# Kernel optimization log

Hardware: AMD Instinct MI355X
Metric: run time of the kernel (lower is better)

Reference implementation:

```python
import jax, jax.numpy as jnp
import numpy as np

B, D = 32, 2048


def setup_inputs() -> dict:
    key = jax.random.key(0)
    ks = jax.random.split(key, 7)
    # torch init: weights ~ N(0, 0.1^2); biases default Linear uniform(-1/sqrt(D), 1/sqrt(D))
    bound = 1.0 / np.sqrt(D)
    return {
        "x": jax.random.normal(ks[0], (B, D), dtype=jnp.float32),
        "Wq": 0.1 * jax.random.normal(ks[1], (D, D), dtype=jnp.float32),
        "bq": jax.random.uniform(ks[2], (D,), minval=-bound, maxval=bound, dtype=jnp.float32),
        "Wk": 0.1 * jax.random.normal(ks[3], (D, D), dtype=jnp.float32),
        "bk": jax.random.uniform(ks[4], (D,), minval=-bound, maxval=bound, dtype=jnp.float32),
        "Wv": 0.1 * jax.random.normal(ks[5], (D, D), dtype=jnp.float32),
        "bv": jax.random.uniform(ks[6], (D,), minval=-bound, maxval=bound, dtype=jnp.float32),
    }


def reference(x, Wq, bq, Wk, bk, Wv, bv):
    # q,k,v: [B, D] feature-wise projections (torch Linear: x @ W^T + b)
    q = x @ Wq.T + bq
    k = x @ Wk.T + bk
    v = x @ Wv.T + bv
    # rank-1 outer product scores[b,i,j] = q[b,i] * k[b,j]  -> [B, D, D]
    scores = q[:, :, None] * k[:, None, :]
    # softmax over dim=1 (as in the original F.softmax(..., dim=1))
    weights = jax.nn.softmax(scores, axis=1)
    # weighted V sum: out[b,i] = sum_j weights[b,i,j] * v[b,j]  -> [B, D]
    out = jnp.einsum("bij,bj->bi", weights, v)
    return out
```

## Files before the change

### kernel.cpp

```cpp
#include <hip/hip_runtime.h>
#include <math.h>


#define D 2048
#define BATCH 32
#define SEG 260

#define XH_OFF  0
#define XL_OFF  32768
#define PA_OFF  65536
#define PB_OFF  262144
#define KDP_OFF 458752
#define NP_OFF  591872

#define L2E 1.4426950408889634f

typedef short s16x8 __attribute__((ext_vector_type(8)));
typedef float f32x4 __attribute__((ext_vector_type(4)));
typedef unsigned short u16;

union FragU { s16x8 v; unsigned u[4]; };

__device__ __forceinline__ float fast_exp2(float x) {
#if __has_builtin(__builtin_amdgcn_exp2f)
  return __builtin_amdgcn_exp2f(x);
#else
  return exp2f(x);
#endif
}
__device__ __forceinline__ u16 f2bf(float f) {
  unsigned u = __float_as_uint(f);
  u = u + 0x7FFFu + ((u >> 16) & 1u);
  return (u16)(u >> 16);
}
__device__ __forceinline__ float bf2f(u16 h) {
  return __uint_as_float(((unsigned)h) << 16);
}
__device__ __forceinline__ void cvt2(float a, float b, unsigned& hp,
                                     unsigned& lp) {
  unsigned ua = __float_as_uint(a), ub = __float_as_uint(b);
  unsigned ha = ua & 0xFFFF0000u, hb = ub & 0xFFFF0000u;
  float la = a - __uint_as_float(ha);
  float lb = b - __uint_as_float(hb);
  hp = (ua >> 16) | hb;
  lp = (__float_as_uint(la) >> 16) | (__float_as_uint(lb) & 0xFFFF0000u);
}

__global__ __launch_bounds__(64) void k0_cvt(const float* __restrict__ x,
                                             float* __restrict__ ws) {
  const int idx = blockIdx.x * 64 + threadIdx.x;
  float4 v = ((const float4*)x)[idx];
  u16* xh = (u16*)(ws + XH_OFF);
  u16* xl = (u16*)(ws + XL_OFF);
  u16 h0 = f2bf(v.x), h1 = f2bf(v.y), h2 = f2bf(v.z), h3 = f2bf(v.w);
  ushort4 hh = {h0, h1, h2, h3};
  ushort4 ll = {f2bf(v.x - bf2f(h0)), f2bf(v.y - bf2f(h1)),
                f2bf(v.z - bf2f(h2)), f2bf(v.w - bf2f(h3))};
  *(ushort4*)(xh + idx * 4) = hh;
  *(ushort4*)(xl + idx * 4) = ll;
}

__global__ __launch_bounds__(256, 3) void k1_proj(
    const float* __restrict__ Wq, const float* __restrict__ Wk,
    const float* __restrict__ Wv, float* __restrict__ ws) {
  __shared__ float red[4][512];
  const int tid = threadIdx.x;
  const int lane = tid & 63, wv = tid >> 6;
  const int tile = blockIdx.x >> 1, kh = blockIdx.x & 1;
  const int r0 = tile * 16;
  const int m = r0 >> 11, lr = r0 & 2047;
  const float* W = (m == 0) ? Wq : (m == 1) ? Wk : Wv;
  const u16* xh = (const u16*)(ws + XH_OFF);
  const u16* xl = (const u16*)(ws + XL_OFF);

  const int kbase = kh * 1024 + wv * 256 + (lane >> 4) * 8;
  const float* ap = W + (size_t)(lr + (lane & 15)) * D + kbase;
  const u16* bh0 = xh + (size_t)(lane & 15) * D + kbase;
  const u16* bl0 = xl + (size_t)(lane & 15) * D + kbase;
  const u16* bh1 = bh0 + 16 * D;
  const u16* bl1 = bl0 + 16 * D;

  f32x4 acc0 = {0.f, 0.f, 0.f, 0.f}, acc1 = {0.f, 0.f, 0.f, 0.f};
#pragma unroll
  for (int s = 0; s < 8; ++s) {
    float4 fa = *(const float4*)(ap + s * 32);
    float4 fb = *(const float4*)(ap + s * 32 + 4);
    s16x8 Bh0 = *(const s16x8*)(bh0 + s * 32);
    s16x8 Bl0 = *(const s16x8*)(bl0 + s * 32);
    s16x8 Bh1 = *(const s16x8*)(bh1 + s * 32);
    s16x8 Bl1 = *(const s16x8*)(bl1 + s * 32);
    FragU Ah, Al;
    cvt2(fa.x, fa.y, Ah.u[0], Al.u[0]);
    cvt2(fa.z, fa.w, Ah.u[1], Al.u[1]);
    cvt2(fb.x, fb.y, Ah.u[2], Al.u[2]);
    cvt2(fb.z, fb.w, Ah.u[3], Al.u[3]);
    acc0 = __builtin_amdgcn_mfma_f32_16x16x32_bf16(Ah.v, Bh0, acc0, 0, 0, 0);
    acc1 = __builtin_amdgcn_mfma_f32_16x16x32_bf16(Ah.v, Bh1, acc1, 0, 0, 0);
    acc0 = __builtin_amdgcn_mfma_f32_16x16x32_bf16(Ah.v, Bl0, acc0, 0, 0, 0);
    acc1 = __builtin_amdgcn_mfma_f32_16x16x32_bf16(Ah.v, Bl1, acc1, 0, 0, 0);
    acc0 = __builtin_amdgcn_mfma_f32_16x16x32_bf16(Al.v, Bh0, acc0, 0, 0, 0);
    acc1 = __builtin_amdgcn_mfma_f32_16x16x32_bf16(Al.v, Bh1, acc1, 0, 0, 0);
  }
  const int col = lane & 15, rq = (lane >> 4) * 4;
#pragma unroll
  for (int r = 0; r < 4; ++r) {
    red[wv][col * 16 + rq + r] = acc0[r];
    red[wv][(col + 16) * 16 + rq + r] = acc1[r];
  }
  __syncthreads();
  float* part = ws + (kh ? PB_OFF : PA_OFF) + (size_t)m * 65536;
#pragma unroll
  for (int i = tid; i < 512; i += 256) {
    float s = (red[0][i] + red[1][i]) + (red[2][i] + red[3][i]);
    part[(size_t)(i >> 4) * D + lr + (i & 15)] = s;
  }
}

__global__ __launch_bounds__(512) void k3_dz(float* __restrict__ ws,
                                             const float* __restrict__ bq,
                                             const float* __restrict__ bk,
                                             const float* __restrict__ bv) {
  __shared__ float qs[2048];
  __shared__ float zs[512];
  __shared__ float rmx[8], rmn[8];
  __shared__ int cnt[2];
  const int bx = blockIdx.x, t = threadIdx.x;
  const int b = bx >> 3, jc = bx & 7;
  if (t == 0) { cnt[0] = 0; cnt[1] = 0; }

  const float* qA = ws + PA_OFF + (size_t)b * D;
  const float* qB = ws + PB_OFF + (size_t)b * D;
  float4 a4 = ((const float4*)qA)[t];
  float4 b4 = ((const float4*)qB)[t];
  float4 c4 = ((const float4*)bq)[t];
  float4 qv = {a4.x + b4.x + c4.x, a4.y + b4.y + c4.y,
               a4.z + b4.z + c4.z, a4.w + b4.w + c4.w};
  *(float4*)&qs[t * 4] = qv;
  float mx = fmaxf(fmaxf(qv.x, qv.y), fmaxf(qv.z, qv.w));
  float mn = fminf(fminf(qv.x, qv.y), fminf(qv.z, qv.w));
#pragma unroll
  for (int off = 32; off; off >>= 1) {
    mx = fmaxf(mx, __shfl_down(mx, off));
    mn = fminf(mn, __shfl_down(mn, off));
  }
  if ((t & 63) == 0) { rmx[t >> 6] = mx; rmn[t >> 6] = mn; }
  __syncthreads();
  mx = rmx[0]; mn = rmn[0];
#pragma unroll
  for (int w = 1; w < 8; ++w) {
    mx = fmaxf(mx, rmx[w]);
    mn = fminf(mn, rmn[w]);
  }

  const int jl = t & 255, ih = t >> 8;
  const size_t jo = (size_t)b * D + jc * 256 + jl;
  const float k2 =
      (ws[PA_OFF + 65536 + jo] + ws[PB_OFF + 65536 + jo] + bk[jc * 256 + jl]) *
      L2E;
  const float m2 = (k2 >= 0.f) ? k2 * mx : k2 * mn;
  const float nm2 = -m2;
  const float* qp = qs + ih * 1024;
  float z0 = 0.f, z1 = 0.f, z2 = 0.f, z3 = 0.f;
#pragma unroll 4
  for (int i = 0; i < 1024; i += 4) {
    float4 q4 = *(const float4*)&qp[i];
    z0 += fast_exp2(fmaf(q4.x, k2, nm2));
    z1 += fast_exp2(fmaf(q4.y, k2, nm2));
    z2 += fast_exp2(fmaf(q4.z, k2, nm2));
    z3 += fast_exp2(fmaf(q4.w, k2, nm2));
  }
  zs[t] = (z0 + z1) + (z2 + z3);
  __syncthreads();

  float2* kdp = (float2*)(ws + KDP_OFF) + ((size_t)b * 8 + jc) * SEG;
  if (t < 256) {
    float Z = zs[t] + zs[t + 256];
    float v =
        ws[PA_OFF + 131072 + jo] + ws[PB_OFF + 131072 + jo] + bv[jc * 256 + jl];
    float d = __log2f(fabsf(v) / Z) - m2;
    int slot;
    if (v >= 0.f) slot = atomicAdd(&cnt[0], 1);
    else          slot = (SEG - 1) - atomicAdd(&cnt[1], 1);
    kdp[slot] = make_float2(k2, d);
  }
  __syncthreads();
  const int npos = cnt[0];
  if (t < 4) kdp[npos + t] = make_float2(0.f, -1e30f);
  if (t == 0) ((int*)(ws + NP_OFF))[b * 8 + jc] = npos;
}

__global__ __launch_bounds__(512) void k4_out(const float* __restrict__ ws,
                                              const float* __restrict__ bq,
                                              float* __restrict__ out) {
  __shared__ float2 kd[8 * SEG];
  __shared__ int np[8];
  __shared__ float rs[512];
  const int bx = blockIdx.x, t = threadIdx.x;
  const int b = bx >> 3, ic = bx & 7;

  const float4* src = (const float4*)((const float2*)(ws + KDP_OFF) +
                                      (size_t)b * 8 * SEG);
  for (int idx = t; idx < (8 * SEG) / 2; idx += 512)
    ((float4*)kd)[idx] = src[idx];
  if (t < 8) np[t] = ((const int*)(ws + NP_OFF))[b * 8 + t];

  const int il = t & 255, jh = t >> 8;
  const int i = ic * 256 + il;
  const size_t io = (size_t)b * D + i;
  const float qi = ws[PA_OFF + io] + ws[PB_OFF + io] + bq[i];
  __syncthreads();

  float p0 = 0.f, p1 = 0.f, p2 = 0.f, p3 = 0.f;
  float n0 = 0.f, n1 = 0.f, n2 = 0.f, n3 = 0.f;
#pragma unroll
  for (int s = jh * 4; s < jh * 4 + 4; ++s) {
    const float2* seg = kd + s * SEG;
    const int npos = np[s];
    const int pe = (npos + 3) & ~3;
    const int ns = (npos + 4) & ~3;
    for (int jj = 0; jj < pe; jj += 4) {
      float4 t0 = *(const float4*)&seg[jj];
      float4 t1 = *(const float4*)&seg[jj + 2];
      p0 += fast_exp2(fmaf(qi, t0.x, t0.y));
      p1 += fast_exp2(fmaf(qi, t0.z, t0.w));
      p2 += fast_exp2(fmaf(qi, t1.x, t1.y));
      p3 += fast_exp2(fmaf(qi, t1.z, t1.w));
    }
    for (int jj = ns; jj < SEG; jj += 4) {
      float4 t0 = *(const float4*)&seg[jj];
      float4 t1 = *(const float4*)&seg[jj + 2];
      n0 += fast_exp2(fmaf(qi, t0.x, t0.y));
      n1 += fast_exp2(fmaf(qi, t0.z, t0.w));
      n2 += fast_exp2(fmaf(qi, t1.x, t1.y));
      n3 += fast_exp2(fmaf(qi, t1.z, t1.w));
    }
  }
  rs[t] = ((p0 + p1) + (p2 + p3)) - ((n0 + n1) + (n2 + n3));
  __syncthreads();
  if (t < 256) out[io] = rs[t] + rs[t + 256];
}

extern "C" void kernel_launch(void* const* d_in, const int* in_sizes, int n_in,
                              void* d_out, int out_size, void* d_ws, size_t ws_size,
                              hipStream_t stream) {
  (void)in_sizes; (void)n_in; (void)out_size; (void)ws_size;
  const float* x  = (const float*)d_in[0];
  const float* Wq = (const float*)d_in[1];
  const float* bq = (const float*)d_in[2];
  const float* Wk = (const float*)d_in[3];
  const float* bk = (const float*)d_in[4];
  const float* Wv = (const float*)d_in[5];
  const float* bv = (const float*)d_in[6];
  float* ws  = (float*)d_ws;
  float* out = (float*)d_out;

  k0_cvt<<<256, 64, 0, stream>>>(x, ws);
  k1_proj<<<768, 256, 0, stream>>>(Wq, Wk, Wv, ws);
  k3_dz<<<256, 512, 0, stream>>>(ws, bq, bk, bv);
  k4_out<<<256, 512, 0, stream>>>(ws, bq, out);
}
```

Baseline: 151.7 us.

## Fuse x conversion into projection, split K four ways, double softmax grid

Drops the separate x-to-bf16 conversion kernel. The projection kernel now loads fp32 x directly and splits it into hi/lo bf16 parts in registers. The projection K dimension is split into four partial sums instead of two, giving twice as many blocks and higher occupancy hints. The dz and output kernels use 16 column chunks per batch instead of 8, so 512 blocks fill the CUs better. This trades one fewer launch and more parallelism for redundant per-block conversion of x, extra partial-sum reads, and smaller segments in the output kernel.

Measured after the change: 143.6 us. 1.06x faster.

```diff
diff --git a/kernel.cpp b/kernel.cpp
--- a/kernel.cpp
+++ b/kernel.cpp
@@ -4,14 +4,11 @@
 
 #define D 2048
 #define BATCH 32
-#define SEG 260
-
-#define XH_OFF  0
-#define XL_OFF  32768
-#define PA_OFF  65536
-#define PB_OFF  262144
-#define KDP_OFF 458752
-#define NP_OFF  591872
+#define SEG 132
+
+#define PART_STRIDE 196608
+#define KDP_OFF 786432
+#define NP_OFF  921600
 
 #define L2E 1.4426950408889634f
 
@@ -27,14 +24,6 @@
 #else
   return exp2f(x);
 #endif
-}
-__device__ __forceinline__ u16 f2bf(float f) {
-  unsigned u = __float_as_uint(f);
-  u = u + 0x7FFFu + ((u >> 16) & 1u);
-  return (u16)(u >> 16);
-}
-__device__ __forceinline__ float bf2f(u16 h) {
-  return __uint_as_float(((unsigned)h) << 16);
 }
 __device__ __forceinline__ void cvt2(float a, float b, unsigned& hp,
                                      unsigned& lp) {
@@ -45,61 +34,50 @@
   hp = (ua >> 16) | hb;
   lp = (__float_as_uint(la) >> 16) | (__float_as_uint(lb) & 0xFFFF0000u);
 }
-
-__global__ __launch_bounds__(64) void k0_cvt(const float* __restrict__ x,
-                                             float* __restrict__ ws) {
-  const int idx = blockIdx.x * 64 + threadIdx.x;
-  float4 v = ((const float4*)x)[idx];
-  u16* xh = (u16*)(ws + XH_OFF);
-  u16* xl = (u16*)(ws + XL_OFF);
-  u16 h0 = f2bf(v.x), h1 = f2bf(v.y), h2 = f2bf(v.z), h3 = f2bf(v.w);
-  ushort4 hh = {h0, h1, h2, h3};
-  ushort4 ll = {f2bf(v.x - bf2f(h0)), f2bf(v.y - bf2f(h1)),
-                f2bf(v.z - bf2f(h2)), f2bf(v.w - bf2f(h3))};
-  *(ushort4*)(xh + idx * 4) = hh;
-  *(ushort4*)(xl + idx * 4) = ll;
-}
-
-__global__ __launch_bounds__(256, 3) void k1_proj(
-    const float* __restrict__ Wq, const float* __restrict__ Wk,
-    const float* __restrict__ Wv, float* __restrict__ ws) {
+__device__ __forceinline__ void cvt8(const float4& fa, const float4& fb,
+                                     FragU& h, FragU& l) {
+  cvt2(fa.x, fa.y, h.u[0], l.u[0]);
+  cvt2(fa.z, fa.w, h.u[1], l.u[1]);
+  cvt2(fb.x, fb.y, h.u[2], l.u[2]);
+  cvt2(fb.z, fb.w, h.u[3], l.u[3]);
+}
+
+__global__ __launch_bounds__(256, 6) void k1_proj(
+    const float* __restrict__ x, const float* __restrict__ Wq,
+    const float* __restrict__ Wk, const float* __restrict__ Wv,
+    float* __restrict__ ws) {
   __shared__ float red[4][512];
   const int tid = threadIdx.x;
   const int lane = tid & 63, wv = tid >> 6;
-  const int tile = blockIdx.x >> 1, kh = blockIdx.x & 1;
-  const int r0 = tile * 16;
-  const int m = r0 >> 11, lr = r0 & 2047;
+  const int tile = blockIdx.x >> 2, kq = blockIdx.x & 3;
+  const int m = tile >> 7, lr = (tile & 127) * 16;
   const float* W = (m == 0) ? Wq : (m == 1) ? Wk : Wv;
-  const u16* xh = (const u16*)(ws + XH_OFF);
-  const u16* xl = (const u16*)(ws + XL_OFF);
-
-  const int kbase = kh * 1024 + wv * 256 + (lane >> 4) * 8;
+
+  const int kbase = kq * 512 + wv * 128 + (lane >> 4) * 8;
   const float* ap = W + (size_t)(lr + (lane & 15)) * D + kbase;
-  const u16* bh0 = xh + (size_t)(lane & 15) * D + kbase;
-  const u16* bl0 = xl + (size_t)(lane & 15) * D + kbase;
-  const u16* bh1 = bh0 + 16 * D;
-  const u16* bl1 = bl0 + 16 * D;
+  const float* xp0 = x + (size_t)(lane & 15) * D + kbase;
+  const float* xp1 = xp0 + 16 * D;
 
   f32x4 acc0 = {0.f, 0.f, 0.f, 0.f}, acc1 = {0.f, 0.f, 0.f, 0.f};
 #pragma unroll
-  for (int s = 0; s < 8; ++s) {
-    float4 fa = *(const float4*)(ap + s * 32);
-    float4 fb = *(const float4*)(ap + s * 32 + 4);
-    s16x8 Bh0 = *(const s16x8*)(bh0 + s * 32);
-    s16x8 Bl0 = *(const s16x8*)(bl0 + s * 32);
-    s16x8 Bh1 = *(const s16x8*)(bh1 + s * 32);
-    s16x8 Bl1 = *(const s16x8*)(bl1 + s * 32);
-    FragU Ah, Al;
-    cvt2(fa.x, fa.y, Ah.u[0], Al.u[0]);
-    cvt2(fa.z, fa.w, Ah.u[1], Al.u[1]);
-    cvt2(fb.x, fb.y, Ah.u[2], Al.u[2]);
-    cvt2(fb.z, fb.w, Ah.u[3], Al.u[3]);
-    acc0 = __builtin_amdgcn_mfma_f32_16x16x32_bf16(Ah.v, Bh0, acc0, 0, 0, 0);
-    acc1 = __builtin_amdgcn_mfma_f32_16x16x32_bf16(Ah.v, Bh1, acc1, 0, 0, 0);
-    acc0 = __builtin_amdgcn_mfma_f32_16x16x32_bf16(Ah.v, Bl0, acc0, 0, 0, 0);
-    acc1 = __builtin_amdgcn_mfma_f32_16x16x32_bf16(Ah.v, Bl1, acc1, 0, 0, 0);
-    acc0 = __builtin_amdgcn_mfma_f32_16x16x32_bf16(Al.v, Bh0, acc0, 0, 0, 0);
-    acc1 = __builtin_amdgcn_mfma_f32_16x16x32_bf16(Al.v, Bh1, acc1, 0, 0, 0);
+  for (int s = 0; s < 4; ++s) {
+    const int off = s * 32;
+    float4 fa = *(const float4*)(ap + off);
+    float4 fb = *(const float4*)(ap + off + 4);
+    float4 x0a = *(const float4*)(xp0 + off);
+    float4 x0b = *(const float4*)(xp0 + off + 4);
+    float4 x1a = *(const float4*)(xp1 + off);
+    float4 x1b = *(const float4*)(xp1 + off + 4);
+    FragU Ah, Al, Bh0, Bl0, Bh1, Bl1;
+    cvt8(fa, fb, Ah, Al);
+    cvt8(x0a, x0b, Bh0, Bl0);
+    cvt8(x1a, x1b, Bh1, Bl1);
+    acc0 = __builtin_amdgcn_mfma_f32_16x16x32_bf16(Ah.v, Bh0.v, acc0, 0, 0, 0);
+    acc1 = __builtin_amdgcn_mfma_f32_16x16x32_bf16(Ah.v, Bh1.v, acc1, 0, 0, 0);
+    acc0 = __builtin_amdgcn_mfma_f32_16x16x32_bf16(Ah.v, Bl0.v, acc0, 0, 0, 0);
+    acc1 = __builtin_amdgcn_mfma_f32_16x16x32_bf16(Ah.v, Bl1.v, acc1, 0, 0, 0);
+    acc0 = __builtin_amdgcn_mfma_f32_16x16x32_bf16(Al.v, Bh0.v, acc0, 0, 0, 0);
+    acc1 = __builtin_amdgcn_mfma_f32_16x16x32_bf16(Al.v, Bh1.v, acc1, 0, 0, 0);
   }
   const int col = lane & 15, rq = (lane >> 4) * 4;
 #pragma unroll
@@ -108,7 +86,7 @@
     red[wv][(col + 16) * 16 + rq + r] = acc1[r];
   }
   __syncthreads();
-  float* part = ws + (kh ? PB_OFF : PA_OFF) + (size_t)m * 65536;
+  float* part = ws + (size_t)kq * PART_STRIDE + (size_t)m * 65536;
 #pragma unroll
   for (int i = tid; i < 512; i += 256) {
     float s = (red[0][i] + red[1][i]) + (red[2][i] + red[3][i]);
@@ -116,25 +94,28 @@
   }
 }
 
-__global__ __launch_bounds__(512) void k3_dz(float* __restrict__ ws,
-                                             const float* __restrict__ bq,
-                                             const float* __restrict__ bk,
-                                             const float* __restrict__ bv) {
+__global__ __launch_bounds__(512, 4) void k3_dz(float* __restrict__ ws,
+                                                const float* __restrict__ bq,
+                                                const float* __restrict__ bk,
+                                                const float* __restrict__ bv) {
   __shared__ float qs[2048];
   __shared__ float zs[512];
   __shared__ float rmx[8], rmn[8];
   __shared__ int cnt[2];
   const int bx = blockIdx.x, t = threadIdx.x;
-  const int b = bx >> 3, jc = bx & 7;
+  const int b = bx >> 4, jc = bx & 15;
   if (t == 0) { cnt[0] = 0; cnt[1] = 0; }
 
-  const float* qA = ws + PA_OFF + (size_t)b * D;
-  const float* qB = ws + PB_OFF + (size_t)b * D;
-  float4 a4 = ((const float4*)qA)[t];
-  float4 b4 = ((const float4*)qB)[t];
-  float4 c4 = ((const float4*)bq)[t];
-  float4 qv = {a4.x + b4.x + c4.x, a4.y + b4.y + c4.y,
-               a4.z + b4.z + c4.z, a4.w + b4.w + c4.w};
+  const size_t qb = (size_t)b * D;
+  float4 p0 = ((const float4*)(ws + qb))[t];
+  float4 p1 = ((const float4*)(ws + PART_STRIDE + qb))[t];
+  float4 p2 = ((const float4*)(ws + 2 * PART_STRIDE + qb))[t];
+  float4 p3 = ((const float4*)(ws + 3 * PART_STRIDE + qb))[t];
+  float4 bb = ((const float4*)bq)[t];
+  float4 qv = {(p0.x + p1.x) + (p2.x + p3.x) + bb.x,
+               (p0.y + p1.y) + (p2.y + p3.y) + bb.y,
+               (p0.z + p1.z) + (p2.z + p3.z) + bb.z,
+               (p0.w + p1.w) + (p2.w + p3.w) + bb.w};
   *(float4*)&qs[t * 4] = qv;
   float mx = fmaxf(fmaxf(qv.x, qv.y), fmaxf(qv.z, qv.w));
   float mn = fminf(fminf(qv.x, qv.y), fminf(qv.z, qv.w));
@@ -152,17 +133,18 @@
     mn = fminf(mn, rmn[w]);
   }
 
-  const int jl = t & 255, ih = t >> 8;
-  const size_t jo = (size_t)b * D + jc * 256 + jl;
-  const float k2 =
-      (ws[PA_OFF + 65536 + jo] + ws[PB_OFF + 65536 + jo] + bk[jc * 256 + jl]) *
-      L2E;
+  const int jl = t & 127, ih = t >> 7;
+  const int j = jc * 128 + jl;
+  const size_t jo = 65536 + (size_t)b * D + j;
+  const float k2 = ((ws[jo] + ws[PART_STRIDE + jo]) +
+                    (ws[2 * PART_STRIDE + jo] + ws[3 * PART_STRIDE + jo]) +
+                    bk[j]) * L2E;
   const float m2 = (k2 >= 0.f) ? k2 * mx : k2 * mn;
   const float nm2 = -m2;
-  const float* qp = qs + ih * 1024;
+  const float* qp = qs + ih * 512;
   float z0 = 0.f, z1 = 0.f, z2 = 0.f, z3 = 0.f;
-#pragma unroll 4
-  for (int i = 0; i < 1024; i += 4) {
+#pragma unroll 8
+  for (int i = 0; i < 512; i += 4) {
     float4 q4 = *(const float4*)&qp[i];
     z0 += fast_exp2(fmaf(q4.x, k2, nm2));
     z1 += fast_exp2(fmaf(q4.y, k2, nm2));
@@ -172,11 +154,12 @@
   zs[t] = (z0 + z1) + (z2 + z3);
   __syncthreads();
 
-  float2* kdp = (float2*)(ws + KDP_OFF) + ((size_t)b * 8 + jc) * SEG;
-  if (t < 256) {
-    float Z = zs[t] + zs[t + 256];
-    float v =
-        ws[PA_OFF + 131072 + jo] + ws[PB_OFF + 131072 + jo] + bv[jc * 256 + jl];
+  float2* kdp = (float2*)(ws + KDP_OFF) + ((size_t)b * 16 + jc) * SEG;
+  if (t < 128) {
+    float Z = (zs[t] + zs[t + 128]) + (zs[t + 256] + zs[t + 384]);
+    const size_t vo = 131072 + (size_t)b * D + j;
+    float v = (ws[vo] + ws[PART_STRIDE + vo]) +
+              (ws[2 * PART_STRIDE + vo] + ws[3 * PART_STRIDE + vo]) + bv[j];
     float d = __log2f(fabsf(v) / Z) - m2;
     int slot;
     if (v >= 0.f) slot = atomicAdd(&cnt[0], 1);
@@ -186,28 +169,30 @@
   __syncthreads();
   const int npos = cnt[0];
   if (t < 4) kdp[npos + t] = make_float2(0.f, -1e30f);
-  if (t == 0) ((int*)(ws + NP_OFF))[b * 8 + jc] = npos;
-}
-
-__global__ __launch_bounds__(512) void k4_out(const float* __restrict__ ws,
-                                              const float* __restrict__ bq,
-                                              float* __restrict__ out) {
-  __shared__ float2 kd[8 * SEG];
-  __shared__ int np[8];
+  if (t == 0) ((int*)(ws + NP_OFF))[b * 16 + jc] = npos;
+}
+
+__global__ __launch_bounds__(512, 4) void k4_out(const float* __restrict__ ws,
+                                                 const float* __restrict__ bq,
+                                                 float* __restrict__ out) {
+  __shared__ float2 kd[16 * SEG];
+  __shared__ int np[16];
   __shared__ float rs[512];
   const int bx = blockIdx.x, t = threadIdx.x;
-  const int b = bx >> 3, ic = bx & 7;
+  const int b = bx >> 4, ic = bx & 15;
 
   const float4* src = (const float4*)((const float2*)(ws + KDP_OFF) +
-                                      (size_t)b * 8 * SEG);
-  for (int idx = t; idx < (8 * SEG) / 2; idx += 512)
+                                      (size_t)b * 16 * SEG);
+  for (int idx = t; idx < (16 * SEG) / 2; idx += 512)
     ((float4*)kd)[idx] = src[idx];
-  if (t < 8) np[t] = ((const int*)(ws + NP_OFF))[b * 8 + t];
-
-  const int il = t & 255, jh = t >> 8;
-  const int i = ic * 256 + il;
+  if (t < 16) np[t] = ((const int*)(ws + NP_OFF))[b * 16 + t];
+
+  const int il = t & 127, jh = t >> 7;
+  const int i = ic * 128 + il;
   const size_t io = (size_t)b * D + i;
-  const float qi = ws[PA_OFF + io] + ws[PB_OFF + io] + bq[i];
+  const float qi = (ws[io] + ws[PART_STRIDE + io]) +
+                   (ws[2 * PART_STRIDE + io] + ws[3 * PART_STRIDE + io]) +
+                   bq[i];
   __syncthreads();
 
   float p0 = 0.f, p1 = 0.f, p2 = 0.f, p3 = 0.f;
@@ -237,7 +222,8 @@
   }
   rs[t] = ((p0 + p1) + (p2 + p3)) - ((n0 + n1) + (n2 + n3));
   __syncthreads();
-  if (t < 256) out[io] = rs[t] + rs[t + 256];
+  if (t < 128)
+    out[io] = (rs[il] + rs[il + 128]) + (rs[il + 256] + rs[il + 384]);
 }
 
 extern "C" void kernel_launch(void* const* d_in, const int* in_sizes, int n_in,
@@ -254,8 +240,7 @@
   float* ws  = (float*)d_ws;
   float* out = (float*)d_out;
 
-  k0_cvt<<<256, 64, 0, stream>>>(x, ws);
-  k1_proj<<<768, 256, 0, stream>>>(Wq, Wk, Wv, ws);
-  k3_dz<<<256, 512, 0, stream>>>(ws, bq, bk, bv);
-  k4_out<<<256, 512, 0, stream>>>(ws, bq, out);
-}
+  k1_proj<<<1536, 256, 0, stream>>>(x, Wq, Wk, Wv, ws);
+  k3_dz<<<512, 512, 0, stream>>>(ws, bq, bk, bv);
+  k4_out<<<512, 512, 0, stream>>>(ws, bq, out);
+}
```
